# Performance work log

Hardware: AMD Instinct MI355X
Metric: run time of the kernel (lower is better)

## Reference

```python
import jax, jax.numpy as jnp
import numpy as np

N_NODES = 50000
N_EDGES = 1600000
IN_FEATS = 128
HID = 128
HEADS = 4
F_HEAD = HID // HEADS  # 32
NEG_SLOPE = 0.2


def setup_inputs() -> dict:
    key = jax.random.key(0)
    ks = jax.random.split(key, 7)
    feat = jax.random.normal(ks[0], (N_NODES, IN_FEATS), dtype=jnp.float32)
    # Xavier-ish scaling for the shared fc weight
    W = jax.random.normal(ks[1], (IN_FEATS, HID), dtype=jnp.float32) * (1.0 / np.sqrt(IN_FEATS))
    attn_l = jax.random.normal(ks[2], (HEADS, F_HEAD), dtype=jnp.float32) * 0.1
    attn_r = jax.random.normal(ks[3], (HEADS, F_HEAD), dtype=jnp.float32) * 0.1
    bias = jnp.zeros((HID,), dtype=jnp.float32)
    src_idx = jax.random.randint(ks[4], (N_EDGES,), 0, N_NODES, dtype=jnp.int32)
    dst_idx = jax.random.randint(ks[5], (N_EDGES,), 0, N_NODES, dtype=jnp.int32)
    return {"feat": feat, "W": W, "attn_l": attn_l, "attn_r": attn_r,
            "bias": bias, "src_idx": src_idx, "dst_idx": dst_idx}


def reference(feat, W, attn_l, attn_r, bias, src_idx, dst_idx):
    N = feat.shape[0]
    # shared linear projection, split into heads: [N, H, F]
    ft = (feat @ W).reshape(N, HEADS, F_HEAD)
    # per-node attention logits: [N, H]
    el = jnp.einsum('nhf,hf->nh', ft, attn_l)
    er = jnp.einsum('nhf,hf->nh', ft, attn_r)
    # per-edge unnormalized score: [E, H]
    e = jax.nn.leaky_relu(el[src_idx] + er[dst_idx], negative_slope=NEG_SLOPE)
    # numerically stable edge softmax grouped by destination node
    m = jax.ops.segment_max(e, dst_idx, num_segments=N)          # [N, H]
    m = jnp.where(jnp.isfinite(m), m, 0.0)                       # guard empty dst
    a = jnp.exp(e - m[dst_idx])                                  # [E, H]
    s = jax.ops.segment_sum(a, dst_idx, num_segments=N)          # [N, H]
    alpha = a / jnp.where(s[dst_idx] > 0, s[dst_idx], 1.0)       # [E, H]
    # weighted scatter-sum aggregation: [N, H, F]
    msgs = ft[src_idx] * alpha[:, :, None]
    out = jax.ops.segment_sum(msgs, dst_idx, num_segments=N)
    out = out + bias.reshape(1, HEADS, F_HEAD)
    return out.reshape(N, HEADS * F_HEAD)  # flatten(1)
```

## Files before the change

kernel.cpp:

```cpp
#include <hip/hip_runtime.h>
#include <hip/hip_bf16.h>
#include <math.h>

#define NEG_SLOPE 0.2f
#define NBMAX 512
#define CAP 8192
#define CH 8192

typedef __attribute__((ext_vector_type(8))) short short8;
typedef __attribute__((ext_vector_type(4))) float f32x4;
union BU { uint4 u; short8 s; };

__device__ __forceinline__ unsigned bf16rne(float f) {
    unsigned u = __float_as_uint(f);
    return (u + 0x7fffu + ((u >> 16) & 1u)) >> 16;
}
__device__ __forceinline__ short bf16s(float f) { return (short)bf16rne(f); }

__global__ void k_zero(int* __restrict__ gh, int NB) {
    int i = blockIdx.x * blockDim.x + threadIdx.x;
    if (i < NB) gh[i] = 0;
}

__global__ __launch_bounds__(256) void k_wprep(
    const float* __restrict__ W, const float* __restrict__ attn_l,
    const float* __restrict__ attn_r, uint4* __restrict__ Wfrag,
    float4* __restrict__ WL, float4* __restrict__ WR) {
    int tid = blockIdx.x * 256 + threadIdx.x;
    if (tid < 2048) {
        int lane = tid & 63;
        int ki = (tid >> 6) & 3;
        int t = (tid >> 8) & 3;
        int cg = tid >> 10;
        int col = cg * 64 + t * 16 + (lane & 15);
        int kb = ki * 32 + (lane >> 4) * 8;
        unsigned d[4];
#pragma unroll
        for (int p = 0; p < 4; ++p) {
            unsigned lo = bf16rne(W[(kb + 2 * p) * 128 + col]);
            unsigned hi = bf16rne(W[(kb + 2 * p + 1) * 128 + col]);
            d[p] = lo | (hi << 16);
        }
        Wfrag[tid] = make_uint4(d[0], d[1], d[2], d[3]);
    } else if (tid < 2048 + 128) {
        int k = tid - 2048;
        const float* wr_ = W + k * 128;
        float l0 = 0, l1 = 0, l2 = 0, l3 = 0, r0 = 0, r1 = 0, r2 = 0, r3 = 0;
        for (int j = 0; j < 32; ++j) {
            l0 += wr_[j] * attn_l[j];
            l1 += wr_[32 + j] * attn_l[32 + j];
            l2 += wr_[64 + j] * attn_l[64 + j];
            l3 += wr_[96 + j] * attn_l[96 + j];
            r0 += wr_[j] * attn_r[j];
            r1 += wr_[32 + j] * attn_r[32 + j];
            r2 += wr_[64 + j] * attn_r[64 + j];
            r3 += wr_[96 + j] * attn_r[96 + j];
        }
        WL[k] = make_float4(l0, l1, l2, l3);
        WR[k] = make_float4(r0, r1, r2, r3);
    }
}

__global__ __launch_bounds__(256) void k_fc(
    const float* __restrict__ feat, const uint4* __restrict__ Wfrag,
    const f32x4* __restrict__ WL, const f32x4* __restrict__ WR,
    unsigned* __restrict__ ftbf, float* __restrict__ el, float* __restrict__ er,
    int N) {
    __shared__ f32x4 WLs[128], WRs[128];
    int tid = threadIdx.x;
    if (tid < 128) WLs[tid] = WL[tid];
    else WRs[tid - 128] = WR[tid - 128];
    __syncthreads();
    const int wave = tid >> 6, lane = tid & 63;
    const int rt = wave & 1, cg = wave >> 1;
    const int nbase = blockIdx.x * 32 + rt * 16;
    const int row = nbase + (lane & 15);
    const int rowc = min(row, N - 1);
    const int q = lane >> 4;

    BU b[4][4];
#pragma unroll
    for (int t = 0; t < 4; ++t)
#pragma unroll
        for (int ki = 0; ki < 4; ++ki)
            b[t][ki].u = Wfrag[cg * 1024 + t * 256 + ki * 64 + lane];

    f32x4 acc0 = {0, 0, 0, 0}, acc1 = {0, 0, 0, 0}, acc2 = {0, 0, 0, 0}, acc3 = {0, 0, 0, 0};
    f32x4 elacc = {0, 0, 0, 0}, eracc = {0, 0, 0, 0};
    const float* fr = feat + (size_t)rowc * 128;
#pragma unroll
    for (int ki = 0; ki < 4; ++ki) {
        float4 f0 = *(const float4*)(fr + ki * 32 + q * 8);
        float4 f1 = *(const float4*)(fr + ki * 32 + q * 8 + 4);
        short8 a;
        a[0] = bf16s(f0.x); a[1] = bf16s(f0.y); a[2] = bf16s(f0.z); a[3] = bf16s(f0.w);
        a[4] = bf16s(f1.x); a[5] = bf16s(f1.y); a[6] = bf16s(f1.z); a[7] = bf16s(f1.w);
        acc0 = __builtin_amdgcn_mfma_f32_16x16x32_bf16(a, b[0][ki].s, acc0, 0, 0, 0);
        acc1 = __builtin_amdgcn_mfma_f32_16x16x32_bf16(a, b[1][ki].s, acc1, 0, 0, 0);
        acc2 = __builtin_amdgcn_mfma_f32_16x16x32_bf16(a, b[2][ki].s, acc2, 0, 0, 0);
        acc3 = __builtin_amdgcn_mfma_f32_16x16x32_bf16(a, b[3][ki].s, acc3, 0, 0, 0);
        if (cg == 0) {
            int kb = ki * 32 + q * 8;
            elacc += f0.x * WLs[kb + 0]; eracc += f0.x * WRs[kb + 0];
            elacc += f0.y * WLs[kb + 1]; eracc += f0.y * WRs[kb + 1];
            elacc += f0.z * WLs[kb + 2]; eracc += f0.z * WRs[kb + 2];
            elacc += f0.w * WLs[kb + 3]; eracc += f0.w * WRs[kb + 3];
            elacc += f1.x * WLs[kb + 4]; eracc += f1.x * WRs[kb + 4];
            elacc += f1.y * WLs[kb + 5]; eracc += f1.y * WRs[kb + 5];
            elacc += f1.z * WLs[kb + 6]; eracc += f1.z * WRs[kb + 6];
            elacc += f1.w * WLs[kb + 7]; eracc += f1.w * WRs[kb + 7];
        }
    }
#pragma unroll
    for (int t = 0; t < 4; ++t) {
#pragma unroll
        for (int r = 0; r < 4; ++r) {
            float d = (t == 0) ? acc0[r] : (t == 1) ? acc1[r] : (t == 2) ? acc2[r] : acc3[r];
            unsigned m = bf16rne(d);
            unsigned nb = (unsigned)__shfl_xor((int)m, 1, 64);
            int node = nbase + q * 4 + r;
            if (!(lane & 1) && node < N)
                ftbf[(size_t)node * 64 + cg * 32 + t * 8 + ((lane & 15) >> 1)] = m | (nb << 16);
        }
    }
    if (cg == 0) {
#pragma unroll
        for (int c = 0; c < 4; ++c) {
            elacc[c] += __shfl_xor(elacc[c], 16, 64);
            eracc[c] += __shfl_xor(eracc[c], 16, 64);
            elacc[c] += __shfl_xor(elacc[c], 32, 64);
            eracc[c] += __shfl_xor(eracc[c], 32, 64);
        }
        if (lane < 16 && row < N) {
            *(float4*)(el + (size_t)row * 4) = make_float4(elacc[0], elacc[1], elacc[2], elacc[3]);
            *(float4*)(er + (size_t)row * 4) = make_float4(eracc[0], eracc[1], eracc[2], eracc[3]);
        }
    }
}

__global__ __launch_bounds__(1024) void k_hist_b(const int* __restrict__ dst,
                                                 int* __restrict__ gh, int E, int NB) {
    __shared__ int h[NBMAX];
    int tid = threadIdx.x;
    for (int t = tid; t < NB; t += 1024) h[t] = 0;
    __syncthreads();
    int beg = blockIdx.x * CH;
    int end = min(beg + CH, E);
    for (int i = beg + tid; i < end; i += 1024) atomicAdd(&h[dst[i] >> 7], 1);
    __syncthreads();
    for (int t = tid; t < NB; t += 1024)
        if (h[t] > 0) atomicAdd(&gh[t], h[t]);
}

__global__ __launch_bounds__(512) void k_scan_b(const int* __restrict__ gh,
                                                int* __restrict__ bucket_off,
                                                int* __restrict__ gcur,
                                                int* __restrict__ offsets,
                                                int E, int N, int NB) {
    __shared__ int ps[512];
    int tid = threadIdx.x;
    int v = (tid < NB) ? gh[tid] : 0;
    ps[tid] = v;
    __syncthreads();
    for (int off = 1; off < 512; off <<= 1) {
        int t = (tid >= off) ? ps[tid - off] : 0;
        __syncthreads();
        ps[tid] += t;
        __syncthreads();
    }
    int excl = ps[tid] - v;
    if (tid < NB) { bucket_off[tid] = excl; gcur[tid] = excl; }
    if (tid == 0) { bucket_off[NB] = E; offsets[N] = E; }
}

__global__ __launch_bounds__(1024) void k_scatter_b(
    const int* __restrict__ src, const int* __restrict__ dst,
    int* __restrict__ gcur, uint2* __restrict__ B, int E, int NB) {
    __shared__ int h[NBMAX];
    __shared__ int lc[NBMAX];
    int tid = threadIdx.x;
    for (int t = tid; t < NB; t += 1024) h[t] = 0;
    __syncthreads();
    int beg = blockIdx.x * CH;
    int end = min(beg + CH, E);
    for (int i = beg + tid; i < end; i += 1024) atomicAdd(&h[dst[i] >> 7], 1);
    __syncthreads();
    for (int t = tid; t < NB; t += 1024)
        lc[t] = (h[t] > 0) ? atomicAdd(&gcur[t], h[t]) : 0;
    __syncthreads();
    for (int i = beg + tid; i < end; i += 1024) {
        int d = dst[i];
        int pos = atomicAdd(&lc[d >> 7], 1);
        B[pos] = make_uint2((unsigned)src[i], (unsigned)d);
    }
}

__global__ __launch_bounds__(512) void k_sort(
    const uint2* __restrict__ B, const int* __restrict__ bucket_off,
    int* __restrict__ src_sorted, int* __restrict__ offsets, int N) {
    __shared__ int h[128];
    __shared__ int c[128];
    __shared__ int outsn[CAP];
    int tid = threadIdx.x;
    int b = blockIdx.x;
    int boff = bucket_off[b];
    int m = bucket_off[b + 1] - boff;
    int base = b << 7;
    if (tid < 128) h[tid] = 0;
    __syncthreads();
    for (int i = tid; i < m; i += 512) atomicAdd(&h[(int)B[boff + i].y - base], 1);
    __syncthreads();
    for (int off = 1; off < 128; off <<= 1) {
        int t = (tid < 128 && tid >= off) ? h[tid - off] : 0;
        __syncthreads();
        if (tid < 128) h[tid] += t;
        __syncthreads();
    }
    if (tid < 128) {
        int excl = tid ? h[tid - 1] : 0;
        c[tid] = excl;
        if (base + tid < N) offsets[base + tid] = boff + excl;
    }
    __syncthreads();
    for (int i = tid; i < m; i += 512) {
        uint2 p = B[boff + i];
        int pos = atomicAdd(&c[(int)p.y - base], 1);
        outsn[pos] = (int)p.x;
    }
    __syncthreads();
    for (int i = tid; i < m; i += 512) src_sorted[boff + i] = outsn[i];
}

__global__ __launch_bounds__(256) void k_aggregate(
    const unsigned int* __restrict__ ftbf, const float* __restrict__ el,
    const float* __restrict__ er, const int* __restrict__ src_sorted,
    const int* __restrict__ offsets, const float* __restrict__ bias,
    float* __restrict__ out, int N) {
    __shared__ float als[4][64][4];
    __shared__ int snl[4][64];
    const int wave = threadIdx.x >> 6;
    const int lane = threadIdx.x & 63;
    const int head = lane >> 4;
    int node = blockIdx.x * 4 + wave;
    if (node >= N) return;
    int beg = offsets[node];
    int end = offsets[node + 1];
    float4 erd = *(const float4*)(er + node * 4);

    float s0 = 0.f, s1 = 0.f, s2 = 0.f, s3 = 0.f;
    float acc0 = 0.f, acc1 = 0.f;
    for (int tile = beg; tile < end; tile += 64) {
        int cnt = min(64, end - tile);
        int sn = 0;
        float a0 = 0.f, a1 = 0.f, a2 = 0.f, a3 = 0.f;
        if (lane < cnt) {
            sn = src_sorted[tile + lane];
            float4 a = *(const float4*)(el + sn * 4);
            float e0 = a.x + erd.x; e0 = fmaxf(e0, NEG_SLOPE * e0);
            float e1 = a.y + erd.y; e1 = fmaxf(e1, NEG_SLOPE * e1);
            float e2 = a.z + erd.z; e2 = fmaxf(e2, NEG_SLOPE * e2);
            float e3 = a.w + erd.w; e3 = fmaxf(e3, NEG_SLOPE * e3);
            a0 = __expf(e0); a1 = __expf(e1);
            a2 = __expf(e2); a3 = __expf(e3);
        }
        s0 += a0; s1 += a1; s2 += a2; s3 += a3;
        *(float4*)(&als[wave][lane][0]) = make_float4(a0, a1, a2, a3);
        snl[wave][lane] = sn;
#pragma unroll 4
        for (int jj = 0; jj < cnt; ++jj) {
            float af = als[wave][jj][head];
            int s = snl[wave][jj];
            unsigned int v = ftbf[(size_t)s * 64 + lane];
            float f0 = __uint_as_float(v << 16);
            float f1 = __uint_as_float(v & 0xffff0000u);
            acc0 = fmaf(f0, af, acc0);
            acc1 = fmaf(f1, af, acc1);
        }
    }
#pragma unroll
    for (int off = 32; off >= 1; off >>= 1) {
        s0 += __shfl_xor(s0, off, 64);
        s1 += __shfl_xor(s1, off, 64);
        s2 += __shfl_xor(s2, off, 64);
        s3 += __shfl_xor(s3, off, 64);
    }
    float ssel = (head == 0) ? s0 : (head == 1) ? s1 : (head == 2) ? s2 : s3;
    float inv = ssel > 0.f ? 1.f / ssel : 0.f;
    float2 b2 = *(const float2*)(bias + 2 * lane);
    float2 o;
    o.x = acc0 * inv + b2.x;
    o.y = acc1 * inv + b2.y;
    *(float2*)(out + (size_t)node * 128 + 2 * lane) = o;
}

extern "C" void kernel_launch(void* const* d_in, const int* in_sizes, int n_in,
                              void* d_out, int out_size, void* d_ws, size_t ws_size,
                              hipStream_t stream) {
    const float* feat = (const float*)d_in[0];
    const float* W = (const float*)d_in[1];
    const float* attn_l = (const float*)d_in[2];
    const float* attn_r = (const float*)d_in[3];
    const float* bias = (const float*)d_in[4];
    const int* src = (const int*)d_in[5];
    const int* dst = (const int*)d_in[6];
    const int N = in_sizes[0] / 128;
    const int E = in_sizes[5];
    const int NB = (N + 127) >> 7;
    float* out = (float*)d_out;

    char* p = (char*)d_ws;
    unsigned int* ftbf = (unsigned int*)p;  p += (size_t)N * 64 * 4;
    uint2* B = (uint2*)p;                   p += (size_t)E * 8;
    float* el = (float*)p;                  p += (size_t)N * 4 * 4;
    float* er = (float*)p;                  p += (size_t)N * 4 * 4;
    int* src_sorted = (int*)p;              p += (size_t)E * 4;
    int* offsets = (int*)p;                 p += ((size_t)(N + 1) * 4 + 15) & ~15ull;
    int* bucket_off = (int*)p;              p += ((size_t)(NB + 1) * 4 + 15) & ~15ull;
    int* gcur = (int*)p;                    p += ((size_t)NB * 4 + 15) & ~15ull;
    int* gh = (int*)p;                      p += ((size_t)NB * 4 + 15) & ~15ull;
    uint4* Wfrag = (uint4*)p;               p += 2048 * 16;
    float4* WL = (float4*)p;                p += 128 * 16;
    float4* WR = (float4*)p;                p += 128 * 16;

    int eblocks = (E + CH - 1) / CH;
    k_zero<<<(NB + 255) / 256, 256, 0, stream>>>(gh, NB);
    k_wprep<<<9, 256, 0, stream>>>(W, attn_l, attn_r, Wfrag, WL, WR);
    k_fc<<<(N + 31) / 32, 256, 0, stream>>>(feat, Wfrag, (const f32x4*)WL,
                                            (const f32x4*)WR, ftbf, el, er, N);
    k_hist_b<<<eblocks, 1024, 0, stream>>>(dst, gh, E, NB);
    k_scan_b<<<1, 512, 0, stream>>>(gh, bucket_off, gcur, offsets, E, N, NB);
    k_scatter_b<<<eblocks, 1024, 0, stream>>>(src, dst, gcur, B, E, NB);
    k_sort<<<NB, 512, 0, stream>>>(B, bucket_off, src_sorted, offsets, N);
    k_aggregate<<<(N + 3) / 4, 256, 0, stream>>>(ftbf, el, er, src_sorted, offsets,
                                                 bias, out, N);
}
```

Baseline: 128.0 us.

## Fuse per-bucket sort with aggregation and pack edge keys into 32 bits

```diff
diff --git a/kernel.cpp b/kernel.cpp
--- a/kernel.cpp
+++ b/kernel.cpp
@@ -3,8 +3,8 @@
 #include <math.h>
 
 #define NEG_SLOPE 0.2f
-#define NBMAX 512
-#define CAP 8192
+#define NBMAX 1024
+#define CAP 4096
 #define CH 8192
 
 typedef __attribute__((ext_vector_type(8))) short short8;
@@ -146,23 +146,22 @@
     __syncthreads();
     int beg = blockIdx.x * CH;
     int end = min(beg + CH, E);
-    for (int i = beg + tid; i < end; i += 1024) atomicAdd(&h[dst[i] >> 7], 1);
+    for (int i = beg + tid; i < end; i += 1024) atomicAdd(&h[dst[i] >> 6], 1);
     __syncthreads();
     for (int t = tid; t < NB; t += 1024)
         if (h[t] > 0) atomicAdd(&gh[t], h[t]);
 }
 
-__global__ __launch_bounds__(512) void k_scan_b(const int* __restrict__ gh,
-                                                int* __restrict__ bucket_off,
-                                                int* __restrict__ gcur,
-                                                int* __restrict__ offsets,
-                                                int E, int N, int NB) {
-    __shared__ int ps[512];
+__global__ __launch_bounds__(1024) void k_scan_b(const int* __restrict__ gh,
+                                                 int* __restrict__ bucket_off,
+                                                 int* __restrict__ gcur,
+                                                 int E, int NB) {
+    __shared__ int ps[1024];
     int tid = threadIdx.x;
     int v = (tid < NB) ? gh[tid] : 0;
     ps[tid] = v;
     __syncthreads();
-    for (int off = 1; off < 512; off <<= 1) {
+    for (int off = 1; off < 1024; off <<= 1) {
         int t = (tid >= off) ? ps[tid - off] : 0;
         __syncthreads();
         ps[tid] += t;
@@ -170,12 +169,12 @@
     }
     int excl = ps[tid] - v;
     if (tid < NB) { bucket_off[tid] = excl; gcur[tid] = excl; }
-    if (tid == 0) { bucket_off[NB] = E; offsets[N] = E; }
+    if (tid == 0) bucket_off[NB] = E;
 }
 
 __global__ __launch_bounds__(1024) void k_scatter_b(
     const int* __restrict__ src, const int* __restrict__ dst,
-    int* __restrict__ gcur, uint2* __restrict__ B, int E, int NB) {
+    int* __restrict__ gcur, unsigned* __restrict__ B, int E, int NB) {
     __shared__ int h[NBMAX];
     __shared__ int lc[NBMAX];
     int tid = threadIdx.x;
@@ -183,114 +182,123 @@
     __syncthreads();
     int beg = blockIdx.x * CH;
     int end = min(beg + CH, E);
-    for (int i = beg + tid; i < end; i += 1024) atomicAdd(&h[dst[i] >> 7], 1);
+    for (int i = beg + tid; i < end; i += 1024) atomicAdd(&h[dst[i] >> 6], 1);
     __syncthreads();
     for (int t = tid; t < NB; t += 1024)
         lc[t] = (h[t] > 0) ? atomicAdd(&gcur[t], h[t]) : 0;
     __syncthreads();
     for (int i = beg + tid; i < end; i += 1024) {
         int d = dst[i];
-        int pos = atomicAdd(&lc[d >> 7], 1);
-        B[pos] = make_uint2((unsigned)src[i], (unsigned)d);
-    }
-}
-
-__global__ __launch_bounds__(512) void k_sort(
-    const uint2* __restrict__ B, const int* __restrict__ bucket_off,
-    int* __restrict__ src_sorted, int* __restrict__ offsets, int N) {
-    __shared__ int h[128];
-    __shared__ int c[128];
+        int pos = atomicAdd(&lc[d >> 6], 1);
+        B[pos] = ((unsigned)src[i] << 6) | (unsigned)(d & 63);
+    }
+}
+
+__global__ __launch_bounds__(512) void k_sortagg(
+    const unsigned* __restrict__ B, const int* __restrict__ bucket_off,
+    const unsigned* __restrict__ ftbf, const float* __restrict__ el,
+    const float* __restrict__ er, const float* __restrict__ bias,
+    float* __restrict__ out, int N) {
+    __shared__ int hist[64];
+    __shared__ int cbeg[65];
+    __shared__ int cur[64];
     __shared__ int outsn[CAP];
-    int tid = threadIdx.x;
-    int b = blockIdx.x;
-    int boff = bucket_off[b];
-    int m = bucket_off[b + 1] - boff;
-    int base = b << 7;
-    if (tid < 128) h[tid] = 0;
-    __syncthreads();
-    for (int i = tid; i < m; i += 512) atomicAdd(&h[(int)B[boff + i].y - base], 1);
-    __syncthreads();
-    for (int off = 1; off < 128; off <<= 1) {
-        int t = (tid < 128 && tid >= off) ? h[tid - off] : 0;
+    __shared__ float als[8][64][4];
+    const int tid = threadIdx.x;
+    const int b = blockIdx.x;
+    const int boff = bucket_off[b];
+    const int m = bucket_off[b + 1] - boff;
+    const int base = b << 6;
+
+    if (tid < 64) hist[tid] = 0;
+    __syncthreads();
+    for (int i = tid; i < m; i += 512) atomicAdd(&hist[B[boff + i] & 63], 1);
+    __syncthreads();
+    int v0 = (tid < 64) ? hist[tid] : 0;
+    for (int off = 1; off < 64; off <<= 1) {
+        int t = (tid < 64 && tid >= off) ? hist[tid - off] : 0;
         __syncthreads();
-        if (tid < 128) h[tid] += t;
+        if (tid < 64) hist[tid] += t;
         __syncthreads();
     }
-    if (tid < 128) {
-        int excl = tid ? h[tid - 1] : 0;
-        c[tid] = excl;
-        if (base + tid < N) offsets[base + tid] = boff + excl;
+    if (tid < 64) {
+        int ex = hist[tid] - v0;
+        cbeg[tid] = ex;
+        cur[tid] = ex;
+        if (tid == 63) cbeg[64] = hist[63];
     }
     __syncthreads();
     for (int i = tid; i < m; i += 512) {
-        uint2 p = B[boff + i];
-        int pos = atomicAdd(&c[(int)p.y - base], 1);
-        outsn[pos] = (int)p.x;
-    }
-    __syncthreads();
-    for (int i = tid; i < m; i += 512) src_sorted[boff + i] = outsn[i];
-}
-
-__global__ __launch_bounds__(256) void k_aggregate(
-    const unsigned int* __restrict__ ftbf, const float* __restrict__ el,
-    const float* __restrict__ er, const int* __restrict__ src_sorted,
-    const int* __restrict__ offsets, const float* __restrict__ bias,
-    float* __restrict__ out, int N) {
-    __shared__ float als[4][64][4];
-    __shared__ int snl[4][64];
-    const int wave = threadIdx.x >> 6;
-    const int lane = threadIdx.x & 63;
-    const int head = lane >> 4;
-    int node = blockIdx.x * 4 + wave;
-    if (node >= N) return;
-    int beg = offsets[node];
-    int end = offsets[node + 1];
-    float4 erd = *(const float4*)(er + node * 4);
-
-    float s0 = 0.f, s1 = 0.f, s2 = 0.f, s3 = 0.f;
-    float acc0 = 0.f, acc1 = 0.f;
-    for (int tile = beg; tile < end; tile += 64) {
-        int cnt = min(64, end - tile);
-        int sn = 0;
-        float a0 = 0.f, a1 = 0.f, a2 = 0.f, a3 = 0.f;
-        if (lane < cnt) {
-            sn = src_sorted[tile + lane];
-            float4 a = *(const float4*)(el + sn * 4);
-            float e0 = a.x + erd.x; e0 = fmaxf(e0, NEG_SLOPE * e0);
-            float e1 = a.y + erd.y; e1 = fmaxf(e1, NEG_SLOPE * e1);
-            float e2 = a.z + erd.z; e2 = fmaxf(e2, NEG_SLOPE * e2);
-            float e3 = a.w + erd.w; e3 = fmaxf(e3, NEG_SLOPE * e3);
-            a0 = __expf(e0); a1 = __expf(e1);
-            a2 = __expf(e2); a3 = __expf(e3);
-        }
-        s0 += a0; s1 += a1; s2 += a2; s3 += a3;
-        *(float4*)(&als[wave][lane][0]) = make_float4(a0, a1, a2, a3);
-        snl[wave][lane] = sn;
+        unsigned p = B[boff + i];
+        int pos = atomicAdd(&cur[p & 63], 1);
+        outsn[pos] = (int)(p >> 6);
+    }
+    __syncthreads();
+
+    const int wave = tid >> 6, lane = tid & 63;
+    const int hl = (lane & 31) >> 3;
+    const int m4 = (lane & 31) << 2;
+    const float4 bv = *(const float4*)(bias + m4);
+
+    for (int nl = wave; nl < 64; nl += 8) {
+        int node = base + nl;
+        if (node >= N) continue;
+        int nb0 = cbeg[nl];
+        int cnt = cbeg[nl + 1] - nb0;
+        float4 erd = *(const float4*)(er + (size_t)node * 4);
+        float s0 = 0.f, s1 = 0.f, s2 = 0.f, s3 = 0.f;
+        float ac0 = 0.f, ac1 = 0.f, ac2 = 0.f, ac3 = 0.f;
+        for (int tile = 0; tile < cnt; tile += 64) {
+            int tc = min(64, cnt - tile);
+            float a0 = 0.f, a1 = 0.f, a2 = 0.f, a3 = 0.f;
+            if (lane < tc) {
+                int sn = outsn[nb0 + tile + lane];
+                float4 a = *(const float4*)(el + (size_t)sn * 4);
+                float e0 = a.x + erd.x; e0 = fmaxf(e0, NEG_SLOPE * e0);
+                float e1 = a.y + erd.y; e1 = fmaxf(e1, NEG_SLOPE * e1);
+                float e2 = a.z + erd.z; e2 = fmaxf(e2, NEG_SLOPE * e2);
+                float e3 = a.w + erd.w; e3 = fmaxf(e3, NEG_SLOPE * e3);
+                a0 = __expf(e0); a1 = __expf(e1);
+                a2 = __expf(e2); a3 = __expf(e3);
+            }
+            s0 += a0; s1 += a1; s2 += a2; s3 += a3;
+            *(float4*)(&als[wave][lane][0]) = make_float4(a0, a1, a2, a3);
 #pragma unroll 4
-        for (int jj = 0; jj < cnt; ++jj) {
-            float af = als[wave][jj][head];
-            int s = snl[wave][jj];
-            unsigned int v = ftbf[(size_t)s * 64 + lane];
-            float f0 = __uint_as_float(v << 16);
-            float f1 = __uint_as_float(v & 0xffff0000u);
-            acc0 = fmaf(f0, af, acc0);
-            acc1 = fmaf(f1, af, acc1);
-        }
-    }
-#pragma unroll
-    for (int off = 32; off >= 1; off >>= 1) {
-        s0 += __shfl_xor(s0, off, 64);
-        s1 += __shfl_xor(s1, off, 64);
-        s2 += __shfl_xor(s2, off, 64);
-        s3 += __shfl_xor(s3, off, 64);
-    }
-    float ssel = (head == 0) ? s0 : (head == 1) ? s1 : (head == 2) ? s2 : s3;
-    float inv = ssel > 0.f ? 1.f / ssel : 0.f;
-    float2 b2 = *(const float2*)(bias + 2 * lane);
-    float2 o;
-    o.x = acc0 * inv + b2.x;
-    o.y = acc1 * inv + b2.y;
-    *(float2*)(out + (size_t)node * 128 + 2 * lane) = o;
+            for (int jj0 = 0; jj0 < tc; jj0 += 2) {
+                int jj = jj0 + (lane >> 5);
+                int j2 = (jj < tc) ? jj : jj0;
+                float af = als[wave][j2][hl];
+                if (jj >= tc) af = 0.f;
+                int sn = outsn[nb0 + tile + j2];
+                uint2 u = *(const uint2*)(ftbf + ((size_t)sn << 6) + ((lane & 31) << 1));
+                ac0 = fmaf(__uint_as_float(u.x << 16), af, ac0);
+                ac1 = fmaf(__uint_as_float(u.x & 0xffff0000u), af, ac1);
+                ac2 = fmaf(__uint_as_float(u.y << 16), af, ac2);
+                ac3 = fmaf(__uint_as_float(u.y & 0xffff0000u), af, ac3);
+            }
+        }
+        ac0 += __shfl_xor(ac0, 32, 64);
+        ac1 += __shfl_xor(ac1, 32, 64);
+        ac2 += __shfl_xor(ac2, 32, 64);
+        ac3 += __shfl_xor(ac3, 32, 64);
+#pragma unroll
+        for (int off = 32; off >= 1; off >>= 1) {
+            s0 += __shfl_xor(s0, off, 64);
+            s1 += __shfl_xor(s1, off, 64);
+            s2 += __shfl_xor(s2, off, 64);
+            s3 += __shfl_xor(s3, off, 64);
+        }
+        float ssel = (hl == 0) ? s0 : (hl == 1) ? s1 : (hl == 2) ? s2 : s3;
+        float inv = ssel > 0.f ? 1.f / ssel : 0.f;
+        if (lane < 32) {
+            float4 o;
+            o.x = ac0 * inv + bv.x;
+            o.y = ac1 * inv + bv.y;
+            o.z = ac2 * inv + bv.z;
+            o.w = ac3 * inv + bv.w;
+            *(float4*)(out + (size_t)node * 128 + m4) = o;
+        }
+    }
 }
 
 extern "C" void kernel_launch(void* const* d_in, const int* in_sizes, int n_in,
@@ -305,16 +313,14 @@
     const int* dst = (const int*)d_in[6];
     const int N = in_sizes[0] / 128;
     const int E = in_sizes[5];
-    const int NB = (N + 127) >> 7;
+    const int NB = (N + 63) >> 6;
     float* out = (float*)d_out;
 
     char* p = (char*)d_ws;
     unsigned int* ftbf = (unsigned int*)p;  p += (size_t)N * 64 * 4;
-    uint2* B = (uint2*)p;                   p += (size_t)E * 8;
+    unsigned* B = (unsigned*)p;             p += ((size_t)E * 4 + 15) & ~15ull;
     float* el = (float*)p;                  p += (size_t)N * 4 * 4;
     float* er = (float*)p;                  p += (size_t)N * 4 * 4;
-    int* src_sorted = (int*)p;              p += (size_t)E * 4;
-    int* offsets = (int*)p;                 p += ((size_t)(N + 1) * 4 + 15) & ~15ull;
     int* bucket_off = (int*)p;              p += ((size_t)(NB + 1) * 4 + 15) & ~15ull;
     int* gcur = (int*)p;                    p += ((size_t)NB * 4 + 15) & ~15ull;
     int* gh = (int*)p;                      p += ((size_t)NB * 4 + 15) & ~15ull;
@@ -328,9 +334,7 @@
     k_fc<<<(N + 31) / 32, 256, 0, stream>>>(feat, Wfrag, (const f32x4*)WL,
                                             (const f32x4*)WR, ftbf, el, er, N);
     k_hist_b<<<eblocks, 1024, 0, stream>>>(dst, gh, E, NB);
-    k_scan_b<<<1, 512, 0, stream>>>(gh, bucket_off, gcur, offsets, E, N, NB);
+    k_scan_b<<<1, 1024, 0, stream>>>(gh, bucket_off, gcur, E, NB);
     k_scatter_b<<<eblocks, 1024, 0, stream>>>(src, dst, gcur, B, E, NB);
-    k_sort<<<NB, 512, 0, stream>>>(B, bucket_off, src_sorted, offsets, N);
-    k_aggregate<<<(N + 3) / 4, 256, 0, stream>>>(ftbf, el, er, src_sorted, offsets,
-                                                 bias, out, N);
-}
+    k_sortagg<<<NB, 512, 0, stream>>>(B, bucket_off, ftbf, el, er, bias, out, N);
+}
```

After: 137.7 us. 7.6% more time.
